# Kernel tuning notes

Measured on AMD Instinct MI355X. Metric: run time of the kernel, lower is better.

The kernel has to match this reference:

```python
import jax, jax.numpy as jnp
import numpy as np

EPS_MASK = 1e-9   # module fills masked scores with eps, NOT -inf
LN_EPS = 1e-5

def _layer_norm(x, g, b):
    mu = jnp.mean(x, axis=-1, keepdims=True)
    var = jnp.mean(jnp.square(x - mu), axis=-1, keepdims=True)
    return (x - mu) * jax.lax.rsqrt(var + LN_EPS) * g + b

def _mha(q_in, k_in, v_in, wq, bq, wk, bk, wv, bv, wo, bo, mask, nhead):
    B, Sq, D = q_in.shape
    dk = D // nhead
    def proj(x, w, b):
        y = x @ w + b                                   # [B,S,D]
        return y.reshape(B, -1, nhead, dk).transpose(0, 2, 1, 3)  # [B,h,S,dk]
    q, k, v = proj(q_in, wq, bq), proj(k_in, wk, bk), proj(v_in, wv, bv)
    scores = jnp.einsum('bhqd,bhkd->bhqk', q, k) / np.sqrt(dk).astype(q.dtype)
    if mask is not None:
        scores = jnp.where(mask[:, None, :, :] == 0, jnp.asarray(EPS_MASK, scores.dtype), scores)
    p = jax.nn.softmax(scores, axis=-1)                 # dropout = identity (eval)
    x = jnp.einsum('bhqk,bhkd->bhqd', p, v)
    x = x.transpose(0, 2, 1, 3).reshape(B, Sq, D)
    return x @ wo + bo

def _forward_post(tgt, memory, tgt_pos, memory_pos, tgt_mask, memory_mask, p):
    nhead = 8
    # self-attention (q=k=tgt+pos, v=tgt)
    q = tgt + tgt_pos
    sa = _mha(q, q, tgt, p['sa_wq'], p['sa_bq'], p['sa_wk'], p['sa_bk'],
              p['sa_wv'], p['sa_bv'], p['sa_wo'], p['sa_bo'], tgt_mask, nhead)
    tgt = _layer_norm(tgt + sa, p['ln1_g'], p['ln1_b'])
    # cross-attention (q=tgt+tgt_pos, k=memory+memory_pos, v=memory)
    mq = tgt + tgt_pos
    mk = memory + memory_pos
    ca = _mha(mq, mk, memory, p['ca_wq'], p['ca_bq'], p['ca_wk'], p['ca_bk'],
              p['ca_wv'], p['ca_bv'], p['ca_wo'], p['ca_bo'], memory_mask, nhead)
    tgt = _layer_norm(tgt + ca, p['ln2_g'], p['ln2_b'])
    # FFN
    h = jax.nn.relu(tgt @ p['mlp_w1'] + p['mlp_b1'])
    ff = h @ p['mlp_w2'] + p['mlp_b2']
    return _layer_norm(tgt + ff, p['ln3_g'], p['ln3_b'])

def setup_inputs() -> dict:
    key = jax.random.key(0)
    B, S, M, D, H = 4, 1024, 1024, 512, 2048
    ks = iter(jax.random.split(key, 40))
    d = {
        'tgt': jax.random.normal(next(ks), (B, S, D), jnp.float32),
        'memory': jax.random.normal(next(ks), (B, M, D), jnp.float32),
        'tgt_pos': jax.random.normal(next(ks), (B, S, D), jnp.float32),
        'memory_pos': jax.random.normal(next(ks), (B, M, D), jnp.float32),
        'tgt_mask': jax.random.randint(next(ks), (B, S, S), 0, 2, jnp.int32),
        'memory_mask': jax.random.randint(next(ks), (B, S, M), 0, 2, jnp.int32),
    }
    for pre in ('sa', 'ca'):
        for nm in ('q', 'k', 'v', 'o'):
            d[f'{pre}_w{nm}'] = jax.random.normal(next(ks), (D, D), jnp.float32) * 0.02
            d[f'{pre}_b{nm}'] = jnp.zeros((D,), jnp.float32)
    for i in (1, 2, 3):
        d[f'ln{i}_g'] = jnp.ones((D,), jnp.float32)
        d[f'ln{i}_b'] = jnp.zeros((D,), jnp.float32)
    d['mlp_w1'] = jax.random.normal(next(ks), (D, H), jnp.float32) * 0.02
    d['mlp_b1'] = jnp.zeros((H,), jnp.float32)
    d['mlp_w2'] = jax.random.normal(next(ks), (H, D), jnp.float32) * 0.02
    d['mlp_b2'] = jnp.zeros((D,), jnp.float32)
    return d

def reference(tgt, memory, tgt_pos, memory_pos, tgt_mask, memory_mask,
              sa_wq, sa_bq, sa_wk, sa_bk, sa_wv, sa_bv, sa_wo, sa_bo,
              ca_wq, ca_bq, ca_wk, ca_bk, ca_wv, ca_bv, ca_wo, ca_bo,
              ln1_g, ln1_b, ln2_g, ln2_b, ln3_g, ln3_b,
              mlp_w1, mlp_b1, mlp_w2, mlp_b2):
    p = dict(sa_wq=sa_wq, sa_bq=sa_bq, sa_wk=sa_wk, sa_bk=sa_bk, sa_wv=sa_wv,
             sa_bv=sa_bv, sa_wo=sa_wo, sa_bo=sa_bo, ca_wq=ca_wq, ca_bq=ca_bq,
             ca_wk=ca_wk, ca_bk=ca_bk, ca_wv=ca_wv, ca_bv=ca_bv, ca_wo=ca_wo,
             ca_bo=ca_bo, ln1_g=ln1_g, ln1_b=ln1_b, ln2_g=ln2_g, ln2_b=ln2_b,
             ln3_g=ln3_g, ln3_b=ln3_b, mlp_w1=mlp_w1, mlp_b1=mlp_b1,
             mlp_w2=mlp_w2, mlp_b2=mlp_b2)
    return _forward_post(tgt, memory, tgt_pos, memory_pos, tgt_mask, memory_mask, p)
```

## Files before the change

### kernel.cpp

```cpp
#include <hip/hip_runtime.h>
#include <stdint.h>

typedef unsigned int u32;
typedef unsigned long long u64;
typedef unsigned short u16;
typedef __attribute__((ext_vector_type(8))) __bf16 bf16x8;
typedef __attribute__((ext_vector_type(4))) float f32x4;

#define DEV __device__ __forceinline__

DEV u16 f2bf(float f) {
    u32 x = __builtin_bit_cast(u32, f);
    u32 r = (x + 0x7FFFu + ((x >> 16) & 1u)) >> 16;
    return (u16)r;
}

DEV float bf2f(u16 x) {
    u32 u = (u32)x << 16;
    return __builtin_bit_cast(float, u);
}

DEV bf16x8 ldg8(const u16* p) {
    return __builtin_bit_cast(bf16x8, *(const uint4*)p);
}

DEV u32 pk2(float a, float b) {
    return (u32)f2bf(a) | ((u32)f2bf(b) << 16);
}

DEV void g2l16(const u16* g, u16* l) {
    __builtin_amdgcn_global_load_lds(
        (const __attribute__((address_space(1))) u32*)g,
        (__attribute__((address_space(3))) u32*)l, 16, 0, 0);
}

DEV f32x4 mfma16(bf16x8 a, bf16x8 b, f32x4 c) {
    return __builtin_amdgcn_mfma_f32_16x16x32_bf16(a, b, c, 0, 0, 0);
}

struct ProArgs {
    const float* w[10];
    u16* wtbase;
    const float4 *tgt, *tpos, *mem, *mpos;
    ushort4 *qin, *tgtb, *memb, *mkb;
    const int4 *m1, *m2;
    u32 *o1, *o2;
};
__global__ __launch_bounds__(256) void prologue_kernel(ProArgs a) {
    const int bx = blockIdx.x, t = threadIdx.x;
    if (bx < 10240) {
        int z = bx >> 10, bxx = bx & 1023;
        int Kd = (z == 9) ? 2048 : 512;
        int Nd = (z == 8) ? 2048 : 512;
        size_t off = (z < 8) ? (size_t)z * 262144
                             : (z == 8 ? (size_t)2097152 : (size_t)3145728);
        u16* out = a.wtbase + off;
        int nx = Nd / 32;
        int txile = bxx % nx, tyile = bxx / nx;
        if (tyile >= Kd / 32) return;
        const float* w = a.w[z];
        __shared__ float tl[32][33];
        int tx = t & 31, ty = t >> 5;
#pragma unroll
        for (int j = 0; j < 4; ++j)
            tl[ty + j * 8][tx] = w[(size_t)(tyile * 32 + ty + j * 8) * Nd + txile * 32 + tx];
        __syncthreads();
#pragma unroll
        for (int j = 0; j < 4; ++j)
            out[(size_t)(txile * 32 + ty + j * 8) * Kd + tyile * 32 + tx] = f2bf(tl[tx][ty + j * 8]);
    } else if (bx < 12288) {
        int i = (bx - 10240) * 256 + t;
        float4 tt = a.tgt[i], p = a.tpos[i], m = a.mem[i], mp = a.mpos[i];
        a.qin[i]  = make_ushort4(f2bf(tt.x + p.x), f2bf(tt.y + p.y), f2bf(tt.z + p.z), f2bf(tt.w + p.w));
        a.tgtb[i] = make_ushort4(f2bf(tt.x), f2bf(tt.y), f2bf(tt.z), f2bf(tt.w));
        a.memb[i] = make_ushort4(f2bf(m.x), f2bf(m.y), f2bf(m.z), f2bf(m.w));
        a.mkb[i]  = make_ushort4(f2bf(m.x + mp.x), f2bf(m.y + mp.y), f2bf(m.z + mp.z), f2bf(m.w + mp.w));
    } else {
        int i = (bx - 12288) * 256 + t;
        const int n8 = 524288;
        bool first = i < n8;
        int idx = first ? i : i - n8;
        const int4* src = first ? a.m1 : a.m2;
        int4 x = src[idx * 2], y = src[idx * 2 + 1];
        u32 by = (u32)(x.x != 0) | ((u32)(x.y != 0) << 1) | ((u32)(x.z != 0) << 2) |
                 ((u32)(x.w != 0) << 3) | ((u32)(y.x != 0) << 4) | ((u32)(y.y != 0) << 5) |
                 ((u32)(y.z != 0) << 6) | ((u32)(y.w != 0) << 7);
        u32 w = by | (__shfl_down(by, 1) << 8) | (__shfl_down(by, 2) << 16) |
                (__shfl_down(by, 3) << 24);
        if ((t & 3) == 0) (first ? a.o1 : a.o2)[idx >> 2] = w;
    }
}

struct GemmSet { const u16* A; const u16* W; const float* bias; void* out; float oscale; int epi; };
struct GemmArgs3 { GemmSet s[3]; };

template <int BM, int BN>
__global__ __launch_bounds__(256) void gemm_kernel(GemmArgs3 args, int M, int N, int Kd) {
    constexpr int MF = BM / 32, NF = BN / 32;
    const GemmSet gs = args.s[blockIdx.z];
    const u16* __restrict__ A = gs.A;
    const u16* __restrict__ W = gs.W;
    const int t = threadIdx.x;
    const int lane = t & 63;
    const int g = lane >> 4, r16 = lane & 15;
    const int wave = t >> 6;
    const int wm = wave >> 1, wn = wave & 1;
    const int nwg = gridDim.x * gridDim.y;
    const int fid = blockIdx.y * gridDim.x + blockIdx.x;
    const int qq = nwg >> 3;
    const int lid = (fid & 7) * qq + (fid >> 3);
    const int m0 = (lid / gridDim.x) * BM, n0 = (lid % gridDim.x) * BN;

    __shared__ __align__(16) u16 As[BM * 64];
    __shared__ __align__(16) u16 Bs[BN * 64];

    f32x4 acc[MF][NF];
#pragma unroll
    for (int m = 0; m < MF; ++m)
#pragma unroll
        for (int n = 0; n < NF; ++n) acc[m][n] = f32x4{0.f, 0.f, 0.f, 0.f};

    for (int kk = 0; kk < Kd; kk += 64) {
        __syncthreads();
#pragma unroll
        for (int i = 0; i < BM / 32; ++i) {
            int cid = t + i * 256, row = cid >> 3, c = cid & 7;
            g2l16(A + (size_t)(m0 + row) * Kd + kk + ((c ^ (row & 7)) << 3), &As[cid << 3]);
        }
#pragma unroll
        for (int i = 0; i < BN / 32; ++i) {
            int cid = t + i * 256, row = cid >> 3, c = cid & 7;
            g2l16(W + (size_t)(n0 + row) * Kd + kk + ((c ^ (row & 7)) << 3), &Bs[cid << 3]);
        }
        __syncthreads();
#pragma unroll
        for (int ks = 0; ks < 2; ++ks) {
            bf16x8 af[MF], bfr[NF];
#pragma unroll
            for (int m = 0; m < MF; ++m) {
                int row = wm * (MF * 16) + m * 16 + r16;
                af[m] = *(const bf16x8*)&As[(row << 6) + (((ks * 4 + g) ^ (row & 7)) << 3)];
            }
#pragma unroll
            for (int n = 0; n < NF; ++n) {
                int row = wn * (NF * 16) + n * 16 + r16;
                bfr[n] = *(const bf16x8*)&Bs[(row << 6) + (((ks * 4 + g) ^ (row & 7)) << 3)];
            }
#pragma unroll
            for (int m = 0; m < MF; ++m)
#pragma unroll
                for (int n = 0; n < NF; ++n)
                    acc[m][n] = mfma16(af[m], bfr[n], acc[m][n]);
        }
    }
    const int epi = gs.epi;
#pragma unroll
    for (int m = 0; m < MF; ++m) {
        int row0 = m0 + wm * (MF * 16) + m * 16 + g * 4;
#pragma unroll
        for (int n = 0; n < NF; ++n) {
            int col = n0 + wn * (NF * 16) + n * 16 + r16;
            float bv = gs.bias[col];
            float v[4];
#pragma unroll
            for (int r = 0; r < 4; ++r) v[r] = (acc[m][n][r] + bv) * gs.oscale;
            if (epi == 1) {
#pragma unroll
                for (int r = 0; r < 4; ++r) v[r] = fmaxf(v[r], 0.f);
            }
            if (epi == 2) {
                float* o = (float*)gs.out;
#pragma unroll
                for (int r = 0; r < 4; ++r) o[(size_t)(row0 + r) * N + col] = v[r];
            } else if (epi == 3) {
                int bb = row0 >> 10, s = row0 & 1023;
                u16* o = (u16*)gs.out +
                         ((size_t)(bb * 8 + (col >> 6)) * 64 + (col & 63)) * 1024 + s;
                *(ushort4*)o = make_ushort4(f2bf(v[0]), f2bf(v[1]), f2bf(v[2]), f2bf(v[3]));
            } else {
                u16* o = (u16*)gs.out;
#pragma unroll
                for (int r = 0; r < 4; ++r) o[(size_t)(row0 + r) * N + col] = f2bf(v[r]);
            }
        }
    }
}

__global__ __launch_bounds__(512) void attn_part_kernel(
    const u16* __restrict__ Q, const u16* __restrict__ K,
    const u16* __restrict__ VT, const u32* __restrict__ mb,
    u16* __restrict__ OP, float2* __restrict__ ML, int Lq, int Lk) {
    const int t = threadIdx.x, lane = t & 63, wave = t >> 6;
    const int g = lane >> 4, r16 = lane & 15;
    const int h = blockIdx.y;
    const int b = blockIdx.z >> 1, p = blockIdx.z & 1;
    const int bh = b * 8 + h;
    const int q0 = blockIdx.x * 128 + wave * 16;
    const int kc0 = p * (Lk >> 1);
    const int NCH = (Lk >> 1) >> 5;

    __shared__ __align__(16) u16 Ks[2][32][64];
    __shared__ __align__(16) u16 Vs[2][64][32];
    __shared__ __align__(16) u16 Pl[8][16][40];

    const size_t qrow = (size_t)b * Lq + q0 + r16;
    const u16* qp = Q + qrow * 512 + h * 64 + g * 8;
    bf16x8 qb0 = ldg8(qp), qb1 = ldg8(qp + 32);
    const u32* mrow = mb + qrow * (Lk >> 5);

    const int sid = t & 255;
    const bool isK = t < 256;
    const int srow = sid >> 3, sc = sid & 7;
    const int vd = sid >> 2, vc = sid & 3;
    const u16* sg = isK
        ? K + (size_t)b * Lk * 512 + h * 64 + (size_t)srow * 512 + ((sc ^ (srow & 7)) << 3)
        : VT + ((size_t)bh * 64 + vd) * Lk + (vc << 3);
    u16* const sl = (isK ? &Ks[0][0][0] : &Vs[0][0][0]) + sid * 8;
    const size_t sstride = isK ? 512 : 1;

    f32x4 acc[4];
#pragma unroll
    for (int dt = 0; dt < 4; ++dt) acc[dt] = f32x4{0.f, 0.f, 0.f, 0.f};
    float mrun = -INFINITY, lrun = 0.f;
    const f32x4 zf = {0.f, 0.f, 0.f, 0.f};

    g2l16(sg + (size_t)kc0 * sstride, sl);
    __syncthreads();

    for (int c = 0; c < NCH; ++c) {
        const int buf = c & 1, nbuf = buf ^ 1;
        const int kc = kc0 + c * 32;
        if (c + 1 < NCH)
            g2l16(sg + (size_t)(kc + 32) * sstride, sl + nbuf * 2048);
        const u16* kb = &Ks[buf][0][0];
        const u16* vb = &Vs[buf][0][0];
        const int r1 = 16 + r16;
        bf16x8 k00 = *(const bf16x8*)(kb + r16 * 64 + ((g ^ (r16 & 7)) << 3));
        bf16x8 k01 = *(const bf16x8*)(kb + r16 * 64 + (((4 + g) ^ (r16 & 7)) << 3));
        bf16x8 k10 = *(const bf16x8*)(kb + r1 * 64 + ((g ^ (r16 & 7)) << 3));
        bf16x8 k11 = *(const bf16x8*)(kb + r1 * 64 + (((4 + g) ^ (r16 & 7)) << 3));
        f32x4 s0 = mfma16(k00, qb0, zf); s0 = mfma16(k01, qb1, s0);
        f32x4 s1 = mfma16(k10, qb0, zf); s1 = mfma16(k11, qb1, s1);

        u32 mw = mrow[kc >> 5];
        float sv[8];
#pragma unroll
        for (int r = 0; r < 4; ++r) {
            sv[r]     = ((mw >> (g * 4 + r)) & 1) ? s0[r] : 1e-9f;
            sv[4 + r] = ((mw >> (16 + g * 4 + r)) & 1) ? s1[r] : 1e-9f;
        }
        float tm = fmaxf(fmaxf(fmaxf(sv[0], sv[1]), fmaxf(sv[2], sv[3])),
                         fmaxf(fmaxf(sv[4], sv[5]), fmaxf(sv[6], sv[7])));
        tm = fmaxf(tm, __shfl_xor(tm, 16));
        tm = fmaxf(tm, __shfl_xor(tm, 32));
        if (!__all(tm <= mrun + 8.f)) {
            float mn = fmaxf(mrun, tm);
            float alpha = __expf(mrun - mn);
            mrun = mn;
            lrun *= alpha;
#pragma unroll
            for (int r = 0; r < 4; ++r) {
                float ar = __shfl(alpha, g * 4 + r);
#pragma unroll
                for (int dt = 0; dt < 4; ++dt) acc[dt][r] *= ar;
            }
        }
        float ts = 0.f;
#pragma unroll
        for (int j = 0; j < 8; ++j) { sv[j] = __expf(sv[j] - mrun); ts += sv[j]; }
        ts += __shfl_xor(ts, 16);
        ts += __shfl_xor(ts, 32);
        lrun += ts;

        uint2 u0; u0.x = pk2(sv[0], sv[1]); u0.y = pk2(sv[2], sv[3]);
        uint2 u1; u1.x = pk2(sv[4], sv[5]); u1.y = pk2(sv[6], sv[7]);
        *(uint2*)&Pl[wave][r16][g * 4] = u0;
        *(uint2*)&Pl[wave][r16][16 + g * 4] = u1;
        bf16x8 pf = *(const bf16x8*)&Pl[wave][r16][g * 8];
#pragma unroll
        for (int dt = 0; dt < 4; ++dt) {
            bf16x8 vf = *(const bf16x8*)(vb + (dt * 16 + r16) * 32 + g * 8);
            acc[dt] = mfma16(pf, vf, acc[dt]);
        }
        __syncthreads();
    }

    if (lane < 16)
        ML[(size_t)p * 32768 + (size_t)bh * 1024 + q0 + lane] = make_float2(mrun, lrun);
    const size_t obase = (size_t)p * 2097152 + ((size_t)bh * 1024 + q0) * 64;
#pragma unroll
    for (int dt = 0; dt < 4; ++dt)
#pragma unroll
        for (int r = 0; r < 4; ++r)
            OP[obase + (size_t)(g * 4 + r) * 64 + dt * 16 + r16] = f2bf(acc[dt][r]);
}

__global__ __launch_bounds__(256) void attn_combine_kernel(
    const u16* __restrict__ OP, const float2* __restrict__ ML, u16* __restrict__ O) {
    int idx = blockIdx.x * 256 + threadIdx.x;
    int row = idx >> 6, d = idx & 63;
    float2 ml0 = ML[row], ml1 = ML[32768 + row];
    float M = fmaxf(ml0.x, ml1.x);
    float w0 = __expf(ml0.x - M), w1 = __expf(ml1.x - M);
    float den = ml0.y * w0 + ml1.y * w1;
    float v = (bf2f(OP[idx]) * w0 + bf2f(OP[2097152 + idx]) * w1) / den;
    int bh = row >> 10, q = row & 1023;
    int b = bh >> 3, h = bh & 7;
    O[((size_t)(b * 1024 + q)) * 512 + h * 64 + d] = f2bf(v);
}

template <int MODE>
__global__ __launch_bounds__(256) void ln_kernel(
    const float* __restrict__ a, const float* __restrict__ bsrc,
    const float* __restrict__ gam, const float* __restrict__ bet,
    const float* __restrict__ pos,
    float* __restrict__ yf, u16* __restrict__ yb, u16* __restrict__ qb) {
    const int lane = threadIdx.x & 63;
    const int row = blockIdx.x * 4 + (threadIdx.x >> 6);
    const size_t base = (size_t)row * 512 + lane * 8;
    float4 av0 = ((const float4*)(a + base))[0];
    float4 av1 = ((const float4*)(a + base))[1];
    float4 bv0 = ((const float4*)(bsrc + base))[0];
    float4 bv1 = ((const float4*)(bsrc + base))[1];
    float x[8] = {av0.x + bv0.x, av0.y + bv0.y, av0.z + bv0.z, av0.w + bv0.w,
                  av1.x + bv1.x, av1.y + bv1.y, av1.z + bv1.z, av1.w + bv1.w};
    float s1 = 0.f, s2 = 0.f;
#pragma unroll
    for (int j = 0; j < 8; ++j) { s1 += x[j]; s2 += x[j] * x[j]; }
#pragma unroll
    for (int d = 1; d < 64; d <<= 1) { s1 += __shfl_xor(s1, d); s2 += __shfl_xor(s2, d); }
    float mean = s1 * (1.f / 512.f);
    float var = s2 * (1.f / 512.f) - mean * mean;
    float rs = rsqrtf(var + 1e-5f);
    float4 gv0 = ((const float4*)(gam + lane * 8))[0];
    float4 gv1 = ((const float4*)(gam + lane * 8))[1];
    float4 be0 = ((const float4*)(bet + lane * 8))[0];
    float4 be1 = ((const float4*)(bet + lane * 8))[1];
    float gg[8] = {gv0.x, gv0.y, gv0.z, gv0.w, gv1.x, gv1.y, gv1.z, gv1.w};
    float bb[8] = {be0.x, be0.y, be0.z, be0.w, be1.x, be1.y, be1.z, be1.w};
    float y[8];
#pragma unroll
    for (int j = 0; j < 8; ++j) y[j] = (x[j] - mean) * rs * gg[j] + bb[j];
    ((float4*)(yf + base))[0] = make_float4(y[0], y[1], y[2], y[3]);
    ((float4*)(yf + base))[1] = make_float4(y[4], y[5], y[6], y[7]);
    if (MODE == 1) {
        ((ushort4*)(yb + base))[0] = make_ushort4(f2bf(y[0]), f2bf(y[1]), f2bf(y[2]), f2bf(y[3]));
        ((ushort4*)(yb + base))[1] = make_ushort4(f2bf(y[4]), f2bf(y[5]), f2bf(y[6]), f2bf(y[7]));
    }
    if (MODE == 0) {
        float4 p0 = ((const float4*)(pos + base))[0];
        float4 p1 = ((const float4*)(pos + base))[1];
        ((ushort4*)(qb + base))[0] = make_ushort4(f2bf(y[0] + p0.x), f2bf(y[1] + p0.y),
                                                  f2bf(y[2] + p0.z), f2bf(y[3] + p0.w));
        ((ushort4*)(qb + base))[1] = make_ushort4(f2bf(y[4] + p1.x), f2bf(y[5] + p1.y),
                                                  f2bf(y[6] + p1.z), f2bf(y[7] + p1.w));
    }
}

extern "C" void kernel_launch(void* const* d_in, const int* in_sizes, int n_in,
                              void* d_out, int out_size, void* d_ws, size_t ws_size,
                              hipStream_t stream) {
    (void)in_sizes; (void)n_in; (void)out_size; (void)ws_size;
    const float* tgt      = (const float*)d_in[0];
    const float* memory   = (const float*)d_in[1];
    const float* tgt_pos  = (const float*)d_in[2];
    const float* mem_pos  = (const float*)d_in[3];
    const int*   tgt_mask = (const int*)d_in[4];
    const int*   mem_mask = (const int*)d_in[5];
    const float* sa_b[4] = {(const float*)d_in[7], (const float*)d_in[9],
                            (const float*)d_in[11], (const float*)d_in[13]};
    const float* ca_b[4] = {(const float*)d_in[15], (const float*)d_in[17],
                            (const float*)d_in[19], (const float*)d_in[21]};
    const float* ln1_g = (const float*)d_in[22]; const float* ln1_b = (const float*)d_in[23];
    const float* ln2_g = (const float*)d_in[24]; const float* ln2_b = (const float*)d_in[25];
    const float* ln3_g = (const float*)d_in[26]; const float* ln3_b = (const float*)d_in[27];
    const float* mlp_b1 = (const float*)d_in[29];
    const float* mlp_b2 = (const float*)d_in[31];

    const size_t MiB = 1024 * 1024;
    char* ws = (char*)d_ws;
    u16*  WT  = (u16*)(ws + 0);
    u32*  MBS = (u32*)(ws + 8 * MiB);
    u32*  MBC = (u32*)(ws + 8 * MiB + 512 * 1024);
    u16*  QIN = (u16*)(ws + 9 * MiB);
    u16*  TGTB= (u16*)(ws + 13 * MiB);
    u16*  MEMB= (u16*)(ws + 17 * MiB);
    u16*  MKB = (u16*)(ws + 21 * MiB);
    u16*  QM  = (u16*)(ws + 25 * MiB);
    u16*  KM  = (u16*)(ws + 29 * MiB);
    u16*  VTM = (u16*)(ws + 37 * MiB);
    u16*  ATNB= (u16*)(ws + 41 * MiB);
    float* PROJ= (float*)(ws + 45 * MiB);
    float* X1F = (float*)(ws + 53 * MiB);
    u16*  MQB = (u16*)(ws + 65 * MiB);
    float* X2F = (float*)(ws + 69 * MiB);
    u16*  X2B = (u16*)(ws + 77 * MiB);
    u16*  FFH = (u16*)(ws + 9 * MiB);
    u16*  OPB = (u16*)(ws + 96 * MiB);
    float2* MLB = (float2*)(ws + 120 * MiB);

    u16* wt[10];
    for (int z = 0; z < 8; ++z) wt[z] = WT + (size_t)z * 262144;
    wt[8] = WT + 2097152;
    wt[9] = WT + 3145728;

    ProArgs pa;
    pa.w[0] = (const float*)d_in[6];  pa.w[1] = (const float*)d_in[8];
    pa.w[2] = (const float*)d_in[10]; pa.w[3] = (const float*)d_in[12];
    pa.w[4] = (const float*)d_in[14]; pa.w[5] = (const float*)d_in[16];
    pa.w[6] = (const float*)d_in[18]; pa.w[7] = (const float*)d_in[20];
    pa.w[8] = (const float*)d_in[28]; pa.w[9] = (const float*)d_in[30];
    pa.wtbase = WT;
    pa.tgt = (const float4*)tgt; pa.tpos = (const float4*)tgt_pos;
    pa.mem = (const float4*)memory; pa.mpos = (const float4*)mem_pos;
    pa.qin = (ushort4*)QIN; pa.tgtb = (ushort4*)TGTB;
    pa.memb = (ushort4*)MEMB; pa.mkb = (ushort4*)MKB;
    pa.m1 = (const int4*)tgt_mask; pa.m2 = (const int4*)mem_mask;
    pa.o1 = MBS; pa.o2 = MBC;
    prologue_kernel<<<16384, 256, 0, stream>>>(pa);

    GemmArgs3 ga;
    ga.s[0] = {QIN,  wt[0], sa_b[0], QM,  0.125f, 0};
    ga.s[1] = {QIN,  wt[1], sa_b[1], KM,  1.f,    0};
    ga.s[2] = {TGTB, wt[2], sa_b[2], VTM, 1.f,    3};
    gemm_kernel<128, 64><<<dim3(8, 32, 3), 256, 0, stream>>>(ga, 4096, 512, 512);
    attn_part_kernel<<<dim3(8, 8, 8), 512, 0, stream>>>(QM, KM, VTM, MBS, OPB, MLB, 1024, 1024);
    attn_combine_kernel<<<8192, 256, 0, stream>>>(OPB, MLB, ATNB);
    ga.s[0] = {ATNB, wt[3], sa_b[3], PROJ, 1.f, 2}; ga.s[1] = ga.s[0]; ga.s[2] = ga.s[0];
    gemm_kernel<64, 64><<<dim3(8, 64, 1), 256, 0, stream>>>(ga, 4096, 512, 512);
    ln_kernel<0><<<1024, 256, 0, stream>>>(tgt, PROJ, ln1_g, ln1_b, tgt_pos, X1F, nullptr, MQB);

    ga.s[0] = {MQB,  wt[4], ca_b[0], QM,  0.125f, 0};
    ga.s[1] = {MKB,  wt[5], ca_b[1], KM,  1.f,    0};
    ga.s[2] = {MEMB, wt[6], ca_b[2], VTM, 1.f,    3};
    gemm_kernel<128, 64><<<dim3(8, 32, 3), 256, 0, stream>>>(ga, 4096, 512, 512);
    attn_part_kernel<<<dim3(8, 8, 8), 512, 0, stream>>>(QM, KM, VTM, MBC, OPB, MLB, 1024, 1024);
    attn_combine_kernel<<<8192, 256, 0, stream>>>(OPB, MLB, ATNB);
    ga.s[0] = {ATNB, wt[7], ca_b[3], PROJ, 1.f, 2}; ga.s[1] = ga.s[0]; ga.s[2] = ga.s[0];
    gemm_kernel<64, 64><<<dim3(8, 64, 1), 256, 0, stream>>>(ga, 4096, 512, 512);
    ln_kernel<1><<<1024, 256, 0, stream>>>(X1F, PROJ, ln2_g, ln2_b, nullptr, X2F, X2B, nullptr);

    ga.s[0] = {X2B, wt[8], mlp_b1, FFH, 1.f, 1}; ga.s[1] = ga.s[0]; ga.s[2] = ga.s[0];
    gemm_kernel<128, 64><<<dim3(32, 32, 1), 256, 0, stream>>>(ga, 4096, 2048, 512);
    ga.s[0] = {FFH, wt[9], mlp_b2, PROJ, 1.f, 2}; ga.s[1] = ga.s[0]; ga.s[2] = ga.s[0];
    gemm_kernel<64, 64><<<dim3(8, 64, 1), 256, 0, stream>>>(ga, 4096, 512, 2048);
    ln_kernel<2><<<1024, 256, 0, stream>>>(X2F, PROJ, ln3_g, ln3_b, nullptr,
                                           (float*)d_out, nullptr, nullptr);
}
```

Before: 184.8 us.

## Store projection outputs as bf16, raise MFMA priority, widen FFN1 tile

The output-projection and FFN2 GEMMs now write bf16 instead of fp32, and the layer-norm kernel reads that bf16 residual input. This halves the intermediate write and read traffic, at the cost of rounding the residual branch to bf16 before the add. Separately, the attention kernel wraps its MFMA blocks in s_setprio to favour matrix issue over other waves. The FFN1 GEMM switches from a 128x64 tile to a 128x128 tile for more reuse per block.

```diff
diff --git a/kernel.cpp b/kernel.cpp
--- a/kernel.cpp
+++ b/kernel.cpp
@@ -168,11 +168,7 @@
 #pragma unroll
                 for (int r = 0; r < 4; ++r) v[r] = fmaxf(v[r], 0.f);
             }
-            if (epi == 2) {
-                float* o = (float*)gs.out;
-#pragma unroll
-                for (int r = 0; r < 4; ++r) o[(size_t)(row0 + r) * N + col] = v[r];
-            } else if (epi == 3) {
+            if (epi == 3) {
                 int bb = row0 >> 10, s = row0 & 1023;
                 u16* o = (u16*)gs.out +
                          ((size_t)(bb * 8 + (col >> 6)) * 64 + (col & 63)) * 1024 + s;
@@ -239,8 +235,10 @@
         bf16x8 k01 = *(const bf16x8*)(kb + r16 * 64 + (((4 + g) ^ (r16 & 7)) << 3));
         bf16x8 k10 = *(const bf16x8*)(kb + r1 * 64 + ((g ^ (r16 & 7)) << 3));
         bf16x8 k11 = *(const bf16x8*)(kb + r1 * 64 + (((4 + g) ^ (r16 & 7)) << 3));
+        __builtin_amdgcn_s_setprio(1);
         f32x4 s0 = mfma16(k00, qb0, zf); s0 = mfma16(k01, qb1, s0);
         f32x4 s1 = mfma16(k10, qb0, zf); s1 = mfma16(k11, qb1, s1);
+        __builtin_amdgcn_s_setprio(0);
 
         u32 mw = mrow[kc >> 5];
         float sv[8];
@@ -277,11 +275,13 @@
         *(uint2*)&Pl[wave][r16][g * 4] = u0;
         *(uint2*)&Pl[wave][r16][16 + g * 4] = u1;
         bf16x8 pf = *(const bf16x8*)&Pl[wave][r16][g * 8];
+        __builtin_amdgcn_s_setprio(1);
 #pragma unroll
         for (int dt = 0; dt < 4; ++dt) {
             bf16x8 vf = *(const bf16x8*)(vb + (dt * 16 + r16) * 32 + g * 8);
             acc[dt] = mfma16(pf, vf, acc[dt]);
         }
+        __builtin_amdgcn_s_setprio(0);
         __syncthreads();
     }
 
@@ -311,7 +311,7 @@
 
 template <int MODE>
 __global__ __launch_bounds__(256) void ln_kernel(
-    const float* __restrict__ a, const float* __restrict__ bsrc,
+    const float* __restrict__ a, const u16* __restrict__ bsrc,
     const float* __restrict__ gam, const float* __restrict__ bet,
     const float* __restrict__ pos,
     float* __restrict__ yf, u16* __restrict__ yb, u16* __restrict__ qb) {
@@ -320,10 +320,11 @@
     const size_t base = (size_t)row * 512 + lane * 8;
     float4 av0 = ((const float4*)(a + base))[0];
     float4 av1 = ((const float4*)(a + base))[1];
-    float4 bv0 = ((const float4*)(bsrc + base))[0];
-    float4 bv1 = ((const float4*)(bsrc + base))[1];
-    float x[8] = {av0.x + bv0.x, av0.y + bv0.y, av0.z + bv0.z, av0.w + bv0.w,
-                  av1.x + bv1.x, av1.y + bv1.y, av1.z + bv1.z, av1.w + bv1.w};
+    uint4 bu = *(const uint4*)(bsrc + base);
+    float x[8] = {av0.x + bf2f((u16)bu.x),        av0.y + bf2f((u16)(bu.x >> 16)),
+                  av0.z + bf2f((u16)bu.y),        av0.w + bf2f((u16)(bu.y >> 16)),
+                  av1.x + bf2f((u16)bu.z),        av1.y + bf2f((u16)(bu.z >> 16)),
+                  av1.z + bf2f((u16)bu.w),        av1.w + bf2f((u16)(bu.w >> 16))};
     float s1 = 0.f, s2 = 0.f;
 #pragma unroll
     for (int j = 0; j < 8; ++j) { s1 += x[j]; s2 += x[j] * x[j]; }
@@ -390,7 +391,7 @@
     u16*  KM  = (u16*)(ws + 29 * MiB);
     u16*  VTM = (u16*)(ws + 37 * MiB);
     u16*  ATNB= (u16*)(ws + 41 * MiB);
-    float* PROJ= (float*)(ws + 45 * MiB);
+    u16*  PROJB = (u16*)(ws + 45 * MiB);
     float* X1F = (float*)(ws + 53 * MiB);
     u16*  MQB = (u16*)(ws + 65 * MiB);
     float* X2F = (float*)(ws + 69 * MiB);
@@ -426,9 +427,9 @@
     gemm_kernel<128, 64><<<dim3(8, 32, 3), 256, 0, stream>>>(ga, 4096, 512, 512);
     attn_part_kernel<<<dim3(8, 8, 8), 512, 0, stream>>>(QM, KM, VTM, MBS, OPB, MLB, 1024, 1024);
     attn_combine_kernel<<<8192, 256, 0, stream>>>(OPB, MLB, ATNB);
-    ga.s[0] = {ATNB, wt[3], sa_b[3], PROJ, 1.f, 2}; ga.s[1] = ga.s[0]; ga.s[2] = ga.s[0];
+    ga.s[0] = {ATNB, wt[3], sa_b[3], PROJB, 1.f, 0}; ga.s[1] = ga.s[0]; ga.s[2] = ga.s[0];
     gemm_kernel<64, 64><<<dim3(8, 64, 1), 256, 0, stream>>>(ga, 4096, 512, 512);
-    ln_kernel<0><<<1024, 256, 0, stream>>>(tgt, PROJ, ln1_g, ln1_b, tgt_pos, X1F, nullptr, MQB);
+    ln_kernel<0><<<1024, 256, 0, stream>>>(tgt, PROJB, ln1_g, ln1_b, tgt_pos, X1F, nullptr, MQB);
 
     ga.s[0] = {MQB,  wt[4], ca_b[0], QM,  0.125f, 0};
     ga.s[1] = {MKB,  wt[5], ca_b[1], KM,  1.f,    0};
@@ -436,14 +437,14 @@
     gemm_kernel<128, 64><<<dim3(8, 32, 3), 256, 0, stream>>>(ga, 4096, 512, 512);
     attn_part_kernel<<<dim3(8, 8, 8), 512, 0, stream>>>(QM, KM, VTM, MBC, OPB, MLB, 1024, 1024);
     attn_combine_kernel<<<8192, 256, 0, stream>>>(OPB, MLB, ATNB);
-    ga.s[0] = {ATNB, wt[7], ca_b[3], PROJ, 1.f, 2}; ga.s[1] = ga.s[0]; ga.s[2] = ga.s[0];
+    ga.s[0] = {ATNB, wt[7], ca_b[3], PROJB, 1.f, 0}; ga.s[1] = ga.s[0]; ga.s[2] = ga.s[0];
     gemm_kernel<64, 64><<<dim3(8, 64, 1), 256, 0, stream>>>(ga, 4096, 512, 512);
-    ln_kernel<1><<<1024, 256, 0, stream>>>(X1F, PROJ, ln2_g, ln2_b, nullptr, X2F, X2B, nullptr);
+    ln_kernel<1><<<1024, 256, 0, stream>>>(X1F, PROJB, ln2_g, ln2_b, nullptr, X2F, X2B, nullptr);
 
     ga.s[0] = {X2B, wt[8], mlp_b1, FFH, 1.f, 1}; ga.s[1] = ga.s[0]; ga.s[2] = ga.s[0];
-    gemm_kernel<128, 64><<<dim3(32, 32, 1), 256, 0, stream>>>(ga, 4096, 2048, 512);
-    ga.s[0] = {FFH, wt[9], mlp_b2, PROJ, 1.f, 2}; ga.s[1] = ga.s[0]; ga.s[2] = ga.s[0];
+    gemm_kernel<128, 128><<<dim3(16, 32, 1), 256, 0, stream>>>(ga, 4096, 2048, 512);
+    ga.s[0] = {FFH, wt[9], mlp_b2, PROJB, 1.f, 0}; ga.s[1] = ga.s[0]; ga.s[2] = ga.s[0];
     gemm_kernel<64, 64><<<dim3(8, 64, 1), 256, 0, stream>>>(ga, 4096, 512, 2048);
-    ln_kernel<2><<<1024, 256, 0, stream>>>(X2F, PROJ, ln3_g, ln3_b, nullptr,
+    ln_kernel<2><<<1024, 256, 0, stream>>>(X2F, PROJB, ln3_g, ln3_b, nullptr,
                                            (float*)d_out, nullptr, nullptr);
 }
```

New measurement: 187.5 us. No clear change (+1.5%).
